# Kernel tuning notes

Hardware: AMD Instinct MI355X
Metric: run time of the kernel (lower is better)

The kernel has to match this reference:

```python
import jax, jax.numpy as jnp
import numpy as np

B = 4096          # number of graphs in the batch
D = 256           # ORB node feature dim (out_dim)
AVG_NODES = 128   # average nodes per graph
N_TOTAL = B * AVG_NODES


def setup_inputs() -> dict:
    key = jax.random.key(0)
    # Ragged per-graph node counts that sum exactly to N_TOTAL.
    rng = np.random.default_rng(0)
    counts = rng.multinomial(N_TOTAL, np.full(B, 1.0 / B))  # ~128 each, all >0 w.h.p.
    n_nodes = jnp.asarray(counts, dtype=jnp.int32)
    node_feats = jax.random.normal(key, (N_TOTAL, D), dtype=jnp.float32)
    return {"node_feats": node_feats, "n_nodes": n_nodes}


def reference(node_feats, n_nodes):
    # Fused segment-mean: one pass over nodes instead of B small kernels.
    n_total = node_feats.shape[0]
    b = n_nodes.shape[0]
    # segment id for every node: [0,0,...,1,1,...,B-1,...]
    seg_ids = jnp.repeat(jnp.arange(b, dtype=jnp.int32), n_nodes,
                         total_repeat_length=n_total)
    sums = jax.ops.segment_sum(node_feats, seg_ids, num_segments=b)  # (B, D)
    graph_feats = sums / n_nodes[:, None].astype(node_feats.dtype)
    return graph_feats
```

## Files before the change

kernel.cpp:

```cpp
#include <hip/hip_runtime.h>


#define BLOCK 256
#define GPB 4

typedef float f4 __attribute__((ext_vector_type(4)));

__global__ __launch_bounds__(BLOCK) void seg_offsets(
    const int* __restrict__ n_nodes, int* __restrict__ offs, int b) {
  __shared__ int part[BLOCK];
  const int t = threadIdx.x;
  const int vpt = (b + BLOCK - 1) / BLOCK;
  const int lo = t * vpt;
  const int hi = min(b, lo + vpt);

  int s = 0;
  for (int i = lo; i < hi; ++i) s += n_nodes[i];
  part[t] = s;
  __syncthreads();

  for (int d = 1; d < BLOCK; d <<= 1) {
    int v = (t >= d) ? part[t - d] : 0;
    __syncthreads();
    part[t] += v;
    __syncthreads();
  }

  int base = (t == 0) ? 0 : part[t - 1];
  for (int i = lo; i < hi; ++i) {
    offs[i] = base;
    base += n_nodes[i];
  }
}

__global__ __launch_bounds__(BLOCK) void seg_mean(
    const float* __restrict__ feats,
    const int* __restrict__ n_nodes,
    const int* __restrict__ offs,
    float* __restrict__ out, int b) {
  const int t = threadIdx.x;
  const int wave = t >> 6;
  const int lane = t & 63;
  const int g = blockIdx.x * GPB + wave;
  if (g >= b) return;

  const int n = n_nodes[g];
  const int start = offs[g];

  const f4* __restrict__ src =
      reinterpret_cast<const f4*>(feats) + (size_t)start * 64 + lane;

  f4 acc[8];
#pragma unroll
  for (int i = 0; i < 8; ++i) acc[i] = (f4)0.0f;

  int r = 0;
  if (n >= 16) {
    f4 buf[8];
#pragma unroll
    for (int i = 0; i < 8; ++i) buf[i] = src[(size_t)i * 64];

    for (r = 8; r + 8 <= n; r += 8) {
      f4 nb[8];
#pragma unroll
      for (int i = 0; i < 8; ++i) nb[i] = src[(size_t)(r + i) * 64];
#pragma unroll
      for (int i = 0; i < 8; ++i) acc[i] += buf[i];
#pragma unroll
      for (int i = 0; i < 8; ++i) buf[i] = nb[i];
    }
#pragma unroll
    for (int i = 0; i < 8; ++i) acc[i] += buf[i];
  }
  for (; r < n; ++r) acc[0] += src[(size_t)r * 64];

  f4 total = ((acc[0] + acc[1]) + (acc[2] + acc[3])) +
             ((acc[4] + acc[5]) + (acc[6] + acc[7]));
  total *= (1.0f / (float)n);

  reinterpret_cast<f4*>(out)[(size_t)g * 64 + lane] = total;
}

extern "C" void kernel_launch(void* const* d_in, const int* in_sizes, int n_in,
                              void* d_out, int out_size, void* d_ws, size_t ws_size,
                              hipStream_t stream) {
  const float* node_feats = (const float*)d_in[0];
  const int* n_nodes = (const int*)d_in[1];
  float* out = (float*)d_out;
  int* offs = (int*)d_ws;

  const int b = in_sizes[1];

  seg_offsets<<<1, BLOCK, 0, stream>>>(n_nodes, offs, b);
  seg_mean<<<(b + GPB - 1) / GPB, BLOCK, 0, stream>>>(node_feats, n_nodes, offs,
                                                      out, b);
}
```

Before: 686.3 us.

## Spread each graph's rows across all waves of a 1024-thread block with LDS reduction

Each 1024-thread block now handles 16 graphs, and every graph's rows are interleaved across all 16 waves instead of one wave owning one graph. Partial sums are combined with LDS atomics, then one wave per graph scales by 1/n and writes the result. Loads use nontemporal hints, and the offsets kernel also writes the end offset so n can be derived from offsets. The aim is to balance ragged work and keep more loads in flight per CU, at the cost of serial per-graph loops inside each wave, LDS atomics and fewer, larger blocks (only 256 blocks).

```diff
diff --git a/kernel.cpp b/kernel.cpp
--- a/kernel.cpp
+++ b/kernel.cpp
@@ -1,16 +1,18 @@
 #include <hip/hip_runtime.h>
 
 
-#define BLOCK 256
-#define GPB 4
+#define BLOCK 1024
+#define WAVES 16
+#define GPB 16
+#define NGP1 (GPB + 1)
 
 typedef float f4 __attribute__((ext_vector_type(4)));
 
-__global__ __launch_bounds__(BLOCK) void seg_offsets(
+__global__ __launch_bounds__(256) void seg_offsets(
     const int* __restrict__ n_nodes, int* __restrict__ offs, int b) {
-  __shared__ int part[BLOCK];
+  __shared__ int part[256];
   const int t = threadIdx.x;
-  const int vpt = (b + BLOCK - 1) / BLOCK;
+  const int vpt = (b + 255) / 256;
   const int lo = t * vpt;
   const int hi = min(b, lo + vpt);
 
@@ -19,7 +21,7 @@
   part[t] = s;
   __syncthreads();
 
-  for (int d = 1; d < BLOCK; d <<= 1) {
+  for (int d = 1; d < 256; d <<= 1) {
     int v = (t >= d) ? part[t - d] : 0;
     __syncthreads();
     part[t] += v;
@@ -31,54 +33,56 @@
     offs[i] = base;
     base += n_nodes[i];
   }
+  if (hi == b && lo < hi) offs[b] = base;
 }
 
-__global__ __launch_bounds__(BLOCK) void seg_mean(
+__global__ __launch_bounds__(BLOCK, 1) void seg_mean(
     const float* __restrict__ feats,
-    const int* __restrict__ n_nodes,
     const int* __restrict__ offs,
     float* __restrict__ out, int b) {
+  __shared__ float lacc[4][GPB][64];
+  __shared__ int loff[NGP1];
+
   const int t = threadIdx.x;
   const int wave = t >> 6;
   const int lane = t & 63;
-  const int g = blockIdx.x * GPB + wave;
-  if (g >= b) return;
+  const int g0 = blockIdx.x * GPB;
 
-  const int n = n_nodes[g];
-  const int start = offs[g];
+  for (int i = t; i < 4 * GPB * 64; i += BLOCK) ((float*)lacc)[i] = 0.0f;
+  if (t < NGP1) loff[t] = offs[min(g0 + t, b)];
+  __syncthreads();
 
-  const f4* __restrict__ src =
-      reinterpret_cast<const f4*>(feats) + (size_t)start * 64 + lane;
+  const int S = loff[0];
+  const f4* __restrict__ srcb = reinterpret_cast<const f4*>(feats);
 
-  f4 acc[8];
-#pragma unroll
-  for (int i = 0; i < 8; ++i) acc[i] = (f4)0.0f;
+  for (int gl = 0; gl < GPB; ++gl) {
+    const int lo = loff[gl], hi = loff[gl + 1];
+    const int rem = (lo - S) & (WAVES - 1);
+    const int r0 = lo + ((wave - rem) & (WAVES - 1));
 
-  int r = 0;
-  if (n >= 16) {
-    f4 buf[8];
-#pragma unroll
-    for (int i = 0; i < 8; ++i) buf[i] = src[(size_t)i * 64];
+    f4 acc = (f4)0.0f;
+#pragma unroll 8
+    for (int r = r0; r < hi; r += WAVES) {
+      acc += __builtin_nontemporal_load(&srcb[(size_t)r * 64 + lane]);
+    }
+    atomicAdd(&lacc[0][gl][lane], acc.x);
+    atomicAdd(&lacc[1][gl][lane], acc.y);
+    atomicAdd(&lacc[2][gl][lane], acc.z);
+    atomicAdd(&lacc[3][gl][lane], acc.w);
+  }
+  __syncthreads();
 
-    for (r = 8; r + 8 <= n; r += 8) {
-      f4 nb[8];
-#pragma unroll
-      for (int i = 0; i < 8; ++i) nb[i] = src[(size_t)(r + i) * 64];
-#pragma unroll
-      for (int i = 0; i < 8; ++i) acc[i] += buf[i];
-#pragma unroll
-      for (int i = 0; i < 8; ++i) buf[i] = nb[i];
-    }
-#pragma unroll
-    for (int i = 0; i < 8; ++i) acc[i] += buf[i];
+  const int g = g0 + wave;
+  if (g < b) {
+    const int n = loff[wave + 1] - loff[wave];
+    f4 tot;
+    tot.x = lacc[0][wave][lane];
+    tot.y = lacc[1][wave][lane];
+    tot.z = lacc[2][wave][lane];
+    tot.w = lacc[3][wave][lane];
+    tot *= (1.0f / (float)n);
+    reinterpret_cast<f4*>(out)[(size_t)g * 64 + lane] = tot;
   }
-  for (; r < n; ++r) acc[0] += src[(size_t)r * 64];
-
-  f4 total = ((acc[0] + acc[1]) + (acc[2] + acc[3])) +
-             ((acc[4] + acc[5]) + (acc[6] + acc[7]));
-  total *= (1.0f / (float)n);
-
-  reinterpret_cast<f4*>(out)[(size_t)g * 64 + lane] = total;
 }
 
 extern "C" void kernel_launch(void* const* d_in, const int* in_sizes, int n_in,
@@ -91,7 +95,6 @@
 
   const int b = in_sizes[1];
 
-  seg_offsets<<<1, BLOCK, 0, stream>>>(n_nodes, offs, b);
-  seg_mean<<<(b + GPB - 1) / GPB, BLOCK, 0, stream>>>(node_feats, n_nodes, offs,
-                                                      out, b);
+  seg_offsets<<<1, 256, 0, stream>>>(n_nodes, offs, b);
+  seg_mean<<<(b + GPB - 1) / GPB, BLOCK, 0, stream>>>(node_feats, offs, out, b);
 }
```

Result: no change. 674.4 us (-1.7%).
